# Performance work log

Measured on AMD Instinct MI355X. Metric: run time of the kernel, lower is better.

Reference implementation:

```python
import jax, jax.numpy as jnp
import numpy as np

EPS = 1e-5


def _lstm(x, W_ih, W_hh, b_ih, b_hh):
    # x: [B, T, in]; torch LSTM gate order i, f, g, o. Returns (last h, last c).
    def step(carry, xt):
        h, c = carry
        z = xt @ W_ih.T + h @ W_hh.T + (b_ih + b_hh)  # [B, 4H]
        i, f, g, o = jnp.split(z, 4, axis=-1)
        c = jax.nn.sigmoid(f) * c + jax.nn.sigmoid(i) * jnp.tanh(g)
        h = jax.nn.sigmoid(o) * jnp.tanh(c)
        return (h, c), None
    h0 = jnp.zeros((x.shape[0], W_hh.shape[1]), x.dtype)
    (h, c), _ = jax.lax.scan(step, (h0, h0), jnp.swapaxes(x, 0, 1))
    return h, c


def _bn_train(x, g, b):
    # BatchNorm1d in training mode: batch stats, biased variance.
    m = x.mean(axis=0)
    v = x.var(axis=0)
    return g * (x - m) * jax.lax.rsqrt(v + EPS) + b


def _forward(agent_traj, neighbours, aW_ih, aW_hh, ab_ih, ab_hh,
             nW_ih, nW_hh, nb_ih, nb_hh, dW_ih, dW_hh, db_ih, db_hh,
             pW, pb, rW, rb, m1W, m1b, g1, be1, m2W, m2b, g2, be2,
             i1W, i1b, ig1, ib1, i2W, i2b, ig2, ib2, segment_ids):
    B = agent_traj.shape[0]
    # relative distance: neighbour last position - owning agent's last position
    rel = neighbours[:, -1, :] - agent_traj[segment_ids, -1, :]          # [N, 2]
    agent_h, agent_c = _lstm(agent_traj, aW_ih, aW_hh, ab_ih, ab_hh)     # [B, 64]
    neigh_h, _ = _lstm(neighbours, nW_ih, nW_hh, nb_ih, nb_hh)           # [N, 64]
    rel_emb = rel @ rW.T + rb                                            # [N, 64]
    x = jnp.concatenate([neigh_h, rel_emb], axis=1)                      # [N, 128]
    x = _bn_train(jax.nn.relu(x @ m1W.T + m1b), g1, be1)                 # [N, 512]
    x = _bn_train(jax.nn.relu(x @ m2W.T + m2b), g2, be2)                 # [N, 1024]
    # per-sample max pooling over each sample's neighbours (zeros if none)
    pooled = jax.ops.segment_max(x, segment_ids, num_segments=B)         # [B, 1024]
    counts = jax.ops.segment_sum(jnp.ones((x.shape[0],), x.dtype), segment_ids, num_segments=B)
    pooled = jnp.where(counts[:, None] > 0, pooled, jnp.zeros((), x.dtype))
    d = jnp.concatenate([pooled, agent_h], axis=1)                       # [B, 1088]
    d = _bn_train(jax.nn.relu(d @ i1W.T + i1b), ig1, ib1)                # [B, 1024]
    d = _bn_train(jax.nn.relu(d @ i2W.T + i2b), ig2, ib2)                # [B, 64]

    def dec_step(carry, _):
        h, c = carry
        z = h @ dW_ih.T + h @ dW_hh.T + (db_ih + db_hh)
        i, f, g, o = jnp.split(z, 4, axis=-1)
        c = jax.nn.sigmoid(f) * c + jax.nn.sigmoid(i) * jnp.tanh(g)
        h = jax.nn.sigmoid(o) * jnp.tanh(c)
        return (h, c), h
    _, hs = jax.lax.scan(dec_step, (d, agent_c), None, length=30)        # [30, B, 64]
    pred = jnp.einsum('tbh,oh->bto', hs, pW) + pb                        # [B, 30, 2]
    return pred


def setup_inputs() -> dict:
    B, T, N, Tn, H = 2048, 20, 32768, 20, 64
    key = jax.random.key(0)
    ki = iter(jax.random.split(key, 40))
    def rn(shape, s=0.1):
        return jax.random.normal(next(ki), shape, dtype=jnp.float32) * s
    inp = dict(
        agent_traj=rn((B, T, 2), 1.0),
        neighbours=rn((N, Tn, 2), 1.0),
        aW_ih=rn((4 * H, 2)), aW_hh=rn((4 * H, H)), ab_ih=rn((4 * H,)), ab_hh=rn((4 * H,)),
        nW_ih=rn((4 * H, 2)), nW_hh=rn((4 * H, H)), nb_ih=rn((4 * H,)), nb_hh=rn((4 * H,)),
        dW_ih=rn((4 * H, H)), dW_hh=rn((4 * H, H)), db_ih=rn((4 * H,)), db_hh=rn((4 * H,)),
        pW=rn((2, H)), pb=rn((2,)),
        rW=rn((H, 2)), rb=rn((H,)),
        m1W=rn((512, 128)), m1b=rn((512,)),
        g1=jnp.ones((512,), jnp.float32), be1=jnp.zeros((512,), jnp.float32),
        m2W=rn((1024, 512)), m2b=rn((1024,)),
        g2=jnp.ones((1024,), jnp.float32), be2=jnp.zeros((1024,), jnp.float32),
        i1W=rn((1024, 1088)), i1b=rn((1024,)),
        ig1=jnp.ones((1024,), jnp.float32), ib1=jnp.zeros((1024,), jnp.float32),
        i2W=rn((H, 1024)), i2b=rn((H,)),
        ig2=jnp.ones((H,), jnp.float32), ib2=jnp.zeros((H,), jnp.float32),
        segment_ids=jnp.sort(jax.random.randint(next(ki), (N,), 0, B)).astype(jnp.int32),
    )
    return inp


def reference(agent_traj, neighbours, aW_ih, aW_hh, ab_ih, ab_hh,
              nW_ih, nW_hh, nb_ih, nb_hh, dW_ih, dW_hh, db_ih, db_hh,
              pW, pb, rW, rb, m1W, m1b, g1, be1, m2W, m2b, g2, be2,
              i1W, i1b, ig1, ib1, i2W, i2b, ig2, ib2, segment_ids):
    return _forward(agent_traj, neighbours, aW_ih, aW_hh, ab_ih, ab_hh,
                    nW_ih, nW_hh, nb_ih, nb_hh, dW_ih, dW_hh, db_ih, db_hh,
                    pW, pb, rW, rb, m1W, m1b, g1, be1, m2W, m2b, g2, be2,
                    i1W, i1b, ig1, ib1, i2W, i2b, ig2, ib2, segment_ids)
```

## Files before the change

### kernel.cpp

```cpp
#include <hip/hip_runtime.h>

#define EPS_BN 1e-5f

typedef __attribute__((ext_vector_type(8))) short short8;
typedef __attribute__((ext_vector_type(4))) float f32x4;

__device__ __forceinline__ float fast_rcp(float x) { return __builtin_amdgcn_rcpf(x); }
__device__ __forceinline__ float sigmoid_f(float x) { return fast_rcp(1.0f + __expf(-x)); }
__device__ __forceinline__ float tanh_f(float x) { return 1.0f - 2.0f * fast_rcp(__expf(2.0f * x) + 1.0f); }

__device__ __forceinline__ unsigned short f2bf(float f) {
    unsigned u = __float_as_uint(f);
    u += 0x7FFFu + ((u >> 16) & 1u);
    return (unsigned short)(u >> 16);
}
__device__ __forceinline__ unsigned pk_bf(float a, float b) {
    return (unsigned)f2bf(a) | ((unsigned)f2bf(b) << 16);
}
__device__ __forceinline__ float bf_hi(float f) {
    return __uint_as_float((unsigned)f2bf(f) << 16);
}
__device__ __forceinline__ float bf2f(unsigned short u) {
    return __uint_as_float((unsigned)u << 16);
}

union AFrag { short e[8]; short8 v; };
union BFrag { uint4 u; short8 v; };

__global__ __launch_bounds__(256, 2) void lstm_mfma(
    const float* __restrict__ x,
    const float* __restrict__ W_ih,
    const float* __restrict__ W_hh,
    const float* __restrict__ b_ih,
    const float* __restrict__ b_hh,
    float* __restrict__ h_out,
    float* __restrict__ c_out,
    int T)
{
    __shared__ unsigned h_ex[2][16 * 52];
    __shared__ float z_lds[4 * 64 * 17];

    const int tid  = threadIdx.x;
    const int g    = tid >> 6;
    const int lane = tid & 63;
    const int s    = lane & 15;
    const int q    = lane >> 4;
    const long seq = (long)blockIdx.x * 16 + s;

    short8 ahi[4][3], alo[4][3];
#pragma unroll
    for (int Ti = 0; Ti < 4; ++Ti) {
        const int n = g * 64 + Ti * 16 + s;
#pragma unroll
        for (int kc = 0; kc < 2; ++kc) {
            const float* src = &W_hh[n * 64 + kc * 32 + q * 8];
            float4 v0 = *(const float4*)src;
            float4 v1 = *(const float4*)(src + 4);
            float v[8] = {v0.x, v0.y, v0.z, v0.w, v1.x, v1.y, v1.z, v1.w};
            AFrag a, b;
#pragma unroll
            for (int j = 0; j < 8; ++j) {
                a.e[j] = (short)f2bf(v[j]);
                b.e[j] = (short)f2bf(v[j] - bf_hi(v[j]));
            }
            ahi[Ti][kc] = a.v;
            alo[Ti][kc] = b.v;
        }
        AFrag a2, b2;
#pragma unroll
        for (int j = 0; j < 8; ++j) { a2.e[j] = 0; b2.e[j] = 0; }
        if (q == 0) {
            const float wi0 = W_ih[n * 2 + 0];
            const float wi1 = W_ih[n * 2 + 1];
            const float bs  = b_ih[n] + b_hh[n];
            a2.e[0] = (short)f2bf(wi0); b2.e[0] = (short)f2bf(wi0 - bf_hi(wi0));
            a2.e[1] = (short)f2bf(wi1); b2.e[1] = (short)f2bf(wi1 - bf_hi(wi1));
            a2.e[2] = (short)f2bf(bs);  b2.e[2] = (short)f2bf(bs  - bf_hi(bs));
        }
        ahi[Ti][2] = a2.v;
        alo[Ti][2] = b2.v;
    }

    for (int i = tid; i < 2 * 16 * 52; i += 256) (&h_ex[0][0])[i] = 0u;
    __syncthreads();
    if (tid < 16) {
        h_ex[0][tid * 52 + 33] = pk_bf(1.0f, 0.0f);
        float2 xv = *(const float2*)&x[((long)blockIdx.x * 16 + tid) * (long)(T * 2)];
        h_ex[0][tid * 52 + 32] = pk_bf(xv.x, xv.y);
        h_ex[1][tid * 52 + 32] = pk_bf(xv.x - bf_hi(xv.x), xv.y - bf_hi(xv.y));
    }
    __syncthreads();

    const int jg = tid >> 4;
    const int sc = tid & 15;
    const long seqc = (long)blockIdx.x * 16 + sc;
    float creg[4] = {0.f, 0.f, 0.f, 0.f};

    for (int t = 0; t < T; ++t) {
        BFrag bhi[3], blo[3];
#pragma unroll
        for (int kc = 0; kc < 3; ++kc) {
            const int off = s * 52 + kc * 16 + (q >> 1) * 8 + (q & 1) * 4;
            bhi[kc].u = *(const uint4*)&h_ex[0][off];
            blo[kc].u = *(const uint4*)&h_ex[1][off];
        }

        f32x4 acc[4];
#pragma unroll
        for (int Ti = 0; Ti < 4; ++Ti) acc[Ti] = (f32x4)0.f;

#pragma unroll
        for (int kc = 0; kc < 3; ++kc) {
            const short8 bh = bhi[kc].v;
            const short8 bl = blo[kc].v;
#pragma unroll
            for (int Ti = 0; Ti < 4; ++Ti) {
                f32x4 a = acc[Ti];
                a = __builtin_amdgcn_mfma_f32_16x16x32_bf16(ahi[Ti][kc], bh, a, 0, 0, 0);
                a = __builtin_amdgcn_mfma_f32_16x16x32_bf16(ahi[Ti][kc], bl, a, 0, 0, 0);
                a = __builtin_amdgcn_mfma_f32_16x16x32_bf16(alo[Ti][kc], bh, a, 0, 0, 0);
                acc[Ti] = a;
            }
        }

#pragma unroll
        for (int Ti = 0; Ti < 4; ++Ti)
#pragma unroll
        for (int r = 0; r < 4; ++r)
            z_lds[(g * 64 + Ti * 16 + q * 4 + r) * 17 + s] = acc[Ti][r];
        __syncthreads();

        float hval[4];
#pragma unroll
        for (int r = 0; r < 4; ++r) {
            const int j = jg * 4 + r;
            const float zi = z_lds[(0 * 64 + j) * 17 + sc];
            const float zf = z_lds[(1 * 64 + j) * 17 + sc];
            const float zg = z_lds[(2 * 64 + j) * 17 + sc];
            const float zo = z_lds[(3 * 64 + j) * 17 + sc];
            const float c = fmaf(sigmoid_f(zf), creg[r], sigmoid_f(zi) * tanh_f(zg));
            creg[r] = c;
            hval[r] = sigmoid_f(zo) * tanh_f(c);
        }
        {
            const int j0 = jg * 4;
            const int w0 = sc * 52 + (j0 >> 4) * 8 + ((j0 >> 2) & 3) * 2;
            h_ex[0][w0]     = pk_bf(hval[0], hval[1]);
            h_ex[0][w0 + 1] = pk_bf(hval[2], hval[3]);
            h_ex[1][w0]     = pk_bf(hval[0] - bf_hi(hval[0]), hval[1] - bf_hi(hval[1]));
            h_ex[1][w0 + 1] = pk_bf(hval[2] - bf_hi(hval[2]), hval[3] - bf_hi(hval[3]));
        }
        if (tid < 16 && t + 1 < T) {
            float2 xv = *(const float2*)&x[((long)blockIdx.x * 16 + tid) * (long)(T * 2) + (t + 1) * 2];
            h_ex[0][tid * 52 + 32] = pk_bf(xv.x, xv.y);
            h_ex[1][tid * 52 + 32] = pk_bf(xv.x - bf_hi(xv.x), xv.y - bf_hi(xv.y));
        }
        if (t == T - 1) {
#pragma unroll
            for (int r = 0; r < 4; ++r) {
                h_out[seqc * 64 + jg * 4 + r] = hval[r];
                if (c_out) c_out[seqc * 64 + jg * 4 + r] = creg[r];
            }
        }
        __syncthreads();
    }
}

__global__ __launch_bounds__(256) void build_x0(
    const float* __restrict__ neigh_h, const float* __restrict__ neighbours,
    const float* __restrict__ agent_traj, const int* __restrict__ seg,
    const float* __restrict__ rW, const float* __restrict__ rb,
    unsigned short* __restrict__ x0hi, unsigned short* __restrict__ x0lo, int T)
{
    const long n = (long)blockIdx.x * 2 + (threadIdx.x >> 7);
    const int j = threadIdx.x & 127;
    float v;
    if (j < 64) {
        v = neigh_h[n*64 + j];
    } else {
        const int o = j - 64;
        const int sid = seg[n];
        const float ra = neighbours[n*(long)(T*2) + (T-1)*2 + 0] - agent_traj[(long)sid*(T*2) + (T-1)*2 + 0];
        const float rbv= neighbours[n*(long)(T*2) + (T-1)*2 + 1] - agent_traj[(long)sid*(T*2) + (T-1)*2 + 1];
        v = fmaf(rW[o*2+0], ra, fmaf(rW[o*2+1], rbv, rb[o]));
    }
    x0hi[n*128 + j] = f2bf(v);
    x0lo[n*128 + j] = f2bf(v - bf_hi(v));
}

__global__ __launch_bounds__(64) void prep_wfrag(
    const float* __restrict__ W, const float* __restrict__ sc, int K,
    unsigned short* __restrict__ Whi, unsigned short* __restrict__ Wlo)
{
    const int nKc = K >> 5;
    const int blk = blockIdx.x;
    const int ti = blk / nKc, kc = blk - ti * nKc;
    const int l = threadIdx.x;
    const int n = ti * 16 + (l & 15);
    const int k0 = kc * 32 + (l >> 4) * 8;
    const long ob = ((long)blk * 64 + l) * 8;
#pragma unroll
    for (int j = 0; j < 8; ++j) {
        float v = W[(long)n * K + k0 + j];
        if (sc) v *= sc[k0 + j];
        Whi[ob + j] = f2bf(v);
        Wlo[ob + j] = f2bf(v - bf_hi(v));
    }
}

__global__ __launch_bounds__(64) void prep_bias(
    const float* __restrict__ W, const float* __restrict__ sh,
    const float* __restrict__ b, int K, float* __restrict__ bout)
{
    const int n = blockIdx.x;
    const int l = threadIdx.x;
    float s = 0.f;
    if (sh)
        for (int k = l; k < K; k += 64) s += sh[k] * W[(long)n * K + k];
#pragma unroll
    for (int m = 32; m >= 1; m >>= 1) s += __shfl_xor(s, m, 64);
    if (l == 0) bout[n] = b[n] + s;
}

__global__ __launch_bounds__(256, 2) void gemm_split(
    const unsigned short* __restrict__ Ahi,
    const unsigned short* __restrict__ Alo,
    const unsigned short* __restrict__ Whi,
    const unsigned short* __restrict__ Wlo,
    const float* __restrict__ bias,
    float* __restrict__ Yf,
    unsigned short* __restrict__ Yhi,
    unsigned short* __restrict__ Ylo,
    float* __restrict__ accum,
    int M, int K, int O)
{
    __shared__ unsigned short As[2][128 * 56];
    const int t = threadIdx.x;
    const int lane = t & 63;
    const int w = t >> 6;
    const int wm = w & 1, wn = w >> 1;
    const int m0 = blockIdx.y * 128, n0 = blockIdx.x * 128;
    const int nKc = K >> 5;

    f32x4 acc[4][4];
#pragma unroll
    for (int mt = 0; mt < 4; ++mt)
#pragma unroll
    for (int nt = 0; nt < 4; ++nt) acc[mt][nt] = (f32x4)0.f;

    const long aoff = (long)(m0 + (t >> 1)) * K + (t & 1) * 16;
    const unsigned short* aph = Ahi + aoff;
    const unsigned short* apl = Alo + aoff;
    const int so = (t >> 1) * 56 + (t & 1) * 16;
    const int arow = wm * 64 + (lane & 15);
    const int acol = (lane >> 4) * 8;
    const long bt0 = (long)((n0 >> 4) + wn * 4);

    uint4 rah0, rah1, ral0, ral1;
    auto loadAreg = [&](int kc) {
        rah0 = *(const uint4*)(aph + kc * 32);
        rah1 = *(const uint4*)(aph + kc * 32 + 8);
        ral0 = *(const uint4*)(apl + kc * 32);
        ral1 = *(const uint4*)(apl + kc * 32 + 8);
    };
    auto storeAs = [&]() {
        *(uint4*)&As[0][so] = rah0; *(uint4*)&As[0][so + 8] = rah1;
        *(uint4*)&As[1][so] = ral0; *(uint4*)&As[1][so + 8] = ral1;
    };
    auto loadB = [&](BFrag* bh, BFrag* bl, int kc) {
#pragma unroll
        for (int nt = 0; nt < 4; ++nt) {
            const long fb = ((bt0 + nt) * nKc + kc) * 512 + lane * 8;
            bh[nt].u = *(const uint4*)(Whi + fb);
            bl[nt].u = *(const uint4*)(Wlo + fb);
        }
    };
    auto compute = [&](BFrag* bh, BFrag* bl) {
        BFrag afh[4], afl[4];
#pragma unroll
        for (int mt = 0; mt < 4; ++mt) {
            afh[mt].u = *(const uint4*)&As[0][(arow + mt * 16) * 56 + acol];
            afl[mt].u = *(const uint4*)&As[1][(arow + mt * 16) * 56 + acol];
        }
#pragma unroll
        for (int nt = 0; nt < 4; ++nt)
#pragma unroll
        for (int mt = 0; mt < 4; ++mt) {
            f32x4 a = acc[mt][nt];
            a = __builtin_amdgcn_mfma_f32_16x16x32_bf16(afh[mt].v, bh[nt].v, a, 0, 0, 0);
            a = __builtin_amdgcn_mfma_f32_16x16x32_bf16(afh[mt].v, bl[nt].v, a, 0, 0, 0);
            a = __builtin_amdgcn_mfma_f32_16x16x32_bf16(afl[mt].v, bh[nt].v, a, 0, 0, 0);
            acc[mt][nt] = a;
        }
    };

    BFrag bh0[4], bl0[4], bh1[4], bl1[4];
    loadAreg(0);
    loadB(bh0, bl0, 0);
    for (int kc = 0; kc < nKc; kc += 2) {
        __syncthreads();
        storeAs();
        loadAreg(kc + 1);
        __syncthreads();
        loadB(bh1, bl1, kc + 1);
        compute(bh0, bl0);
        __syncthreads();
        storeAs();
        if (kc + 2 < nKc) loadAreg(kc + 2);
        __syncthreads();
        if (kc + 2 < nKc) loadB(bh0, bl0, kc + 2);
        compute(bh1, bl1);
    }

    const int cn = lane & 15, cq = lane >> 4;
#pragma unroll
    for (int nt = 0; nt < 4; ++nt) {
        const int n = n0 + wn * 64 + nt * 16 + cn;
        const float bs = bias[n];
        float s = 0.f, ssq = 0.f;
#pragma unroll
        for (int mt = 0; mt < 4; ++mt)
#pragma unroll
        for (int r = 0; r < 4; ++r) {
            const long m = m0 + wm * 64 + mt * 16 + cq * 4 + r;
            const float v = fmaxf(acc[mt][nt][r] + bs, 0.f);
            s += v; ssq += v * v;
            if (Yf) {
                Yf[m * O + n] = v;
            } else {
                Yhi[m * O + n] = f2bf(v);
                Ylo[m * O + n] = f2bf(v - bf_hi(v));
            }
        }
        if (accum) {
            s   += __shfl_xor(s, 16, 64);   ssq += __shfl_xor(ssq, 16, 64);
            s   += __shfl_xor(s, 32, 64);   ssq += __shfl_xor(ssq, 32, 64);
            if (cq == 0) {
                atomicAdd(&accum[n], s);
                atomicAdd(&accum[O + n], ssq);
            }
        }
    }
}

__global__ __launch_bounds__(256) void colstats(
    const float* __restrict__ Y, int M, int O, int chunkRows,
    float* __restrict__ accum)
{
    const int c = blockIdx.x * 64 + (threadIdx.x & 63);
    const int rgrp = threadIdx.x >> 6;
    const int r0 = blockIdx.y * chunkRows;
    int rend = r0 + chunkRows; if (rend > M) rend = M;
    float s = 0.f, ss = 0.f;
    for (int r = r0 + rgrp; r < rend; r += 4) {
        const float v = Y[(long)r*O + c];
        s += v; ss += v*v;
    }
    __shared__ float l1[256], l2[256];
    l1[threadIdx.x] = s; l2[threadIdx.x] = ss;
    __syncthreads();
    if (threadIdx.x < 64) {
        const int c2 = blockIdx.x * 64 + threadIdx.x;
        s  = l1[threadIdx.x] + l1[threadIdx.x+64] + l1[threadIdx.x+128] + l1[threadIdx.x+192];
        ss = l2[threadIdx.x] + l2[threadIdx.x+64] + l2[threadIdx.x+128] + l2[threadIdx.x+192];
        atomicAdd(&accum[c2], s);
        atomicAdd(&accum[O + c2], ss);
    }
}

__global__ __launch_bounds__(256) void bn_finalize(
    const float* __restrict__ accum, const float* __restrict__ g,
    const float* __restrict__ be, int O, float invM,
    float* __restrict__ scale, float* __restrict__ shift)
{
    const int o = blockIdx.x * 256 + threadIdx.x;
    if (o < O) {
        const float mean = accum[o] * invM;
        const float var  = accum[O + o] * invM - mean * mean;
        const float sc   = g[o] * rsqrtf(var + EPS_BN);
        scale[o] = sc;
        shift[o] = be[o] - mean * sc;
    }
}

__global__ __launch_bounds__(256) void segmax_kernel(
    const float* __restrict__ Y , const int* __restrict__ seg,
    const float* __restrict__ scale, const float* __restrict__ shift,
    int N, float* __restrict__ pooled )
{
    const int b = blockIdx.x;
    int l = 0, h = N;
    while (l < h) { const int mid = (l + h) >> 1; if (seg[mid] < b) l = mid + 1; else h = mid; }
    const int lo = l;
    h = N;
    while (l < h) { const int mid = (l + h) >> 1; if (seg[mid] < b + 1) l = mid + 1; else h = mid; }
    const int hi = l;

    for (int cc = threadIdx.x; cc < 1024; cc += 256) {
        float m;
        if (lo >= hi) {
            m = 0.0f;
        } else {
            m = -3.4e38f;
            for (int r = lo; r < hi; ++r) m = fmaxf(m, Y[(long)r*1024 + cc]);
            m = fmaf(scale[cc], m, shift[cc]);
        }
        pooled[(long)b*1024 + cc] = m;
    }
}

__global__ __launch_bounds__(256) void build_d0(
    const float* __restrict__ pooled, const float* __restrict__ agent_h,
    unsigned short* __restrict__ d0hi, unsigned short* __restrict__ d0lo)
{
    const int b = blockIdx.x;
    for (int c = threadIdx.x; c < 1088; c += 256) {
        const float v = (c < 1024) ? pooled[(long)b*1024 + c]
                                   : agent_h[(long)b*64 + (c - 1024)];
        d0hi[(long)b*1088 + c] = f2bf(v);
        d0lo[(long)b*1088 + c] = f2bf(v - bf_hi(v));
    }
}

__global__ __launch_bounds__(256) void gemm_i2_part(
    const float* __restrict__ A,
    const float* __restrict__ W,
    const float* __restrict__ ascale, const float* __restrict__ ashift,
    float* __restrict__ part, int M, int K, int kchunk)
{
    __shared__ float As[16][132];
    __shared__ float Bs[16][68];
    const int t = threadIdx.x;
    const int m0 = blockIdx.x * 128;
    const int ks = blockIdx.y;
    const int kbeg = ks * kchunk;
    const int kend = kbeg + kchunk;
    const int tm = (t & 15) * 8;
    const int tn = (t >> 4) * 4;
    const int ar = t >> 1;
    const int ac = (t & 1) * 8;
    const int br = t >> 2;
    const int bc = (t & 3) * 4;

    float acc[8][4];
#pragma unroll
    for (int i = 0; i < 8; ++i)
#pragma unroll
    for (int j = 0; j < 4; ++j) acc[i][j] = 0.f;

    for (int k0 = kbeg; k0 < kend; k0 += 16) {
        float4 a0 = *(const float4*)&A[(long)(m0+ar)*K + k0 + ac];
        float4 a1 = *(const float4*)&A[(long)(m0+ar)*K + k0 + ac + 4];
        float4 s0 = *(const float4*)&ascale[k0 + ac];
        float4 s1 = *(const float4*)&ascale[k0 + ac + 4];
        float4 h0 = *(const float4*)&ashift[k0 + ac];
        float4 h1 = *(const float4*)&ashift[k0 + ac + 4];
        a0.x = fmaf(a0.x, s0.x, h0.x); a0.y = fmaf(a0.y, s0.y, h0.y);
        a0.z = fmaf(a0.z, s0.z, h0.z); a0.w = fmaf(a0.w, s0.w, h0.w);
        a1.x = fmaf(a1.x, s1.x, h1.x); a1.y = fmaf(a1.y, s1.y, h1.y);
        a1.z = fmaf(a1.z, s1.z, h1.z); a1.w = fmaf(a1.w, s1.w, h1.w);
        float4 b0 = *(const float4*)&W[(long)br*K + k0 + bc];
        __syncthreads();
        As[ac+0][ar] = a0.x; As[ac+1][ar] = a0.y; As[ac+2][ar] = a0.z; As[ac+3][ar] = a0.w;
        As[ac+4][ar] = a1.x; As[ac+5][ar] = a1.y; As[ac+6][ar] = a1.z; As[ac+7][ar] = a1.w;
        Bs[bc+0][br] = b0.x; Bs[bc+1][br] = b0.y; Bs[bc+2][br] = b0.z; Bs[bc+3][br] = b0.w;
        __syncthreads();
#pragma unroll
        for (int kk = 0; kk < 16; ++kk) {
            float av[8], bv[4];
            *(float4*)&av[0] = *(const float4*)&As[kk][tm];
            *(float4*)&av[4] = *(const float4*)&As[kk][tm + 4];
            *(float4*)&bv[0] = *(const float4*)&Bs[kk][tn];
#pragma unroll
            for (int i = 0; i < 8; ++i)
#pragma unroll
            for (int j = 0; j < 4; ++j)
                acc[i][j] = fmaf(av[i], bv[j], acc[i][j]);
        }
    }

    float* po = part + (long)ks * M * 64;
#pragma unroll
    for (int i = 0; i < 8; ++i)
        *(float4*)&po[(long)(m0 + tm + i) * 64 + tn] = *(float4*)&acc[i][0];
}

__global__ __launch_bounds__(256) void i2_finish(
    const float* __restrict__ part, const float* __restrict__ bias,
    int M, int KS, float* __restrict__ t2)
{
    const long idx = (long)blockIdx.x * 256 + threadIdx.x;
    if (idx < (long)M * 64) {
        float s = 0.f;
        for (int ks = 0; ks < KS; ++ks) s += part[(long)ks * M * 64 + idx];
        t2[idx] = fmaxf(s + bias[idx & 63], 0.f);
    }
}

__global__ __launch_bounds__(256) void prep_dec(
    const float* __restrict__ dW_ih, const float* __restrict__ dW_hh,
    const float* __restrict__ db_ih, const float* __restrict__ db_hh,
    float* __restrict__ Wc, float* __restrict__ bc)
{
    const int idx = blockIdx.x * 256 + threadIdx.x;
    if (idx < 256*64) Wc[idx] = dW_ih[idx] + dW_hh[idx];
    else if (idx < 256*64 + 256) bc[idx - 256*64] = db_ih[idx - 256*64] + db_hh[idx - 256*64];
}

__global__ __launch_bounds__(256) void decoder_kernel(
    const float* __restrict__ t2, const float* __restrict__ sc4,
    const float* __restrict__ sh4, const float* __restrict__ agent_c,
    const float* __restrict__ Wc, const float* __restrict__ bc,
    const float* __restrict__ pW, const float* __restrict__ pb,
    float* __restrict__ pred )
{
    __shared__ float h_lds[2][64];
    __shared__ float zg_lds[2][64];
    __shared__ float zo_lds[2][64];
    const int t = threadIdx.x;
    const int lane = t & 63;
    const int wave = t >> 6;
    const int s = wave >> 1;
    const int role = wave & 1;
    const long seq = (long)blockIdx.x * 2 + s;

    const int r0 = role * 128 + lane;
    const int r1 = r0 + 64;
    float w0[64], w1[64];
#pragma unroll
    for (int k = 0; k < 64; k += 4) {
        float4 va = *(const float4*)&Wc[r0 * 64 + k];
        w0[k] = va.x; w0[k+1] = va.y; w0[k+2] = va.z; w0[k+3] = va.w;
        float4 vb = *(const float4*)&Wc[r1 * 64 + k];
        w1[k] = vb.x; w1[k+1] = vb.y; w1[k+2] = vb.z; w1[k+3] = vb.w;
    }
    const float bias0 = bc[r0];
    const float bias1 = bc[r1];
    const float pw0 = pW[lane], pw1 = pW[64 + lane];
    const float pb0 = pb[0], pb1 = pb[1];

    float c = agent_c[seq*64 + lane];
    if (role == 0)
        h_lds[s][lane] = fmaf(sc4[lane], t2[seq*64 + lane], sh4[lane]);
    __syncthreads();
    float hv = h_lds[s][lane];

    for (int step = 0; step < 30; ++step) {
        float z0 = bias0, z1 = bias1;
#pragma unroll
        for (int k = 0; k < 64; ++k) {
            float hk = __int_as_float(__builtin_amdgcn_readlane(__float_as_int(hv), k));
            z0 = fmaf(hk, w0[k], z0);
            z1 = fmaf(hk, w1[k], z1);
        }
        if (role == 1) { zg_lds[s][lane] = z0; zo_lds[s][lane] = z1; }
        __syncthreads();
        if (role == 0) {
            const float ig = sigmoid_f(z0);
            const float fg = sigmoid_f(z1);
            const float gg = tanh_f(zg_lds[s][lane]);
            const float og = sigmoid_f(zo_lds[s][lane]);
            c = fmaf(fg, c, ig * gg);
            h_lds[s][lane] = og * tanh_f(c);
        }
        __syncthreads();
        hv = h_lds[s][lane];
        if (role == 0) {
            float p0 = hv * pw0;
            float p1 = hv * pw1;
#pragma unroll
            for (int m = 32; m >= 1; m >>= 1) {
                p0 += __shfl_xor(p0, m, 64);
                p1 += __shfl_xor(p1, m, 64);
            }
            if (lane == 0) {
                pred[seq*60 + step*2 + 0] = p0 + pb0;
                pred[seq*60 + step*2 + 1] = p1 + pb1;
            }
        }
    }
}

extern "C" void kernel_launch(void* const* d_in, const int* in_sizes, int n_in,
                              void* d_out, int out_size, void* d_ws, size_t ws_size,
                              hipStream_t stream)
{
    const float* agent_traj = (const float*)d_in[0];
    const float* neighbours = (const float*)d_in[1];
    const float* aW_ih = (const float*)d_in[2];
    const float* aW_hh = (const float*)d_in[3];
    const float* ab_ih = (const float*)d_in[4];
    const float* ab_hh = (const float*)d_in[5];
    const float* nW_ih = (const float*)d_in[6];
    const float* nW_hh = (const float*)d_in[7];
    const float* nb_ih = (const float*)d_in[8];
    const float* nb_hh = (const float*)d_in[9];
    const float* dW_ih = (const float*)d_in[10];
    const float* dW_hh = (const float*)d_in[11];
    const float* db_ih = (const float*)d_in[12];
    const float* db_hh = (const float*)d_in[13];
    const float* pW = (const float*)d_in[14];
    const float* pb = (const float*)d_in[15];
    const float* rW = (const float*)d_in[16];
    const float* rb = (const float*)d_in[17];
    const float* m1W = (const float*)d_in[18];
    const float* m1b = (const float*)d_in[19];
    const float* g1  = (const float*)d_in[20];
    const float* be1 = (const float*)d_in[21];
    const float* m2W = (const float*)d_in[22];
    const float* m2b = (const float*)d_in[23];
    const float* g2  = (const float*)d_in[24];
    const float* be2 = (const float*)d_in[25];
    const float* i1W = (const float*)d_in[26];
    const float* i1b = (const float*)d_in[27];
    const float* ig1 = (const float*)d_in[28];
    const float* ib1 = (const float*)d_in[29];
    const float* i2W = (const float*)d_in[30];
    const float* i2b = (const float*)d_in[31];
    const float* ig2 = (const float*)d_in[32];
    const float* ib2 = (const float*)d_in[33];
    const int*   seg = (const int*)d_in[34];
    float* pred = (float*)d_out;

    const int B = 2048, T = 20, N = 32768;

    char* p = (char*)d_ws;
    auto alloc = [&](size_t bytes) -> char* {
        char* r = p; p += (bytes + 255) & ~(size_t)255; return r;
    };
    float* agent_h = (float*)alloc((size_t)B*64*4);
    float* agent_c = (float*)alloc((size_t)B*64*4);
    char* neigh_region = alloc((size_t)N*64*4);
    char* x0hi_region  = alloc((size_t)N*128*2);
    unsigned short* x0lo = (unsigned short*)alloc((size_t)N*128*2);
    char* y1hi_region  = alloc((size_t)N*512*2);
    unsigned short* y1lo = (unsigned short*)alloc((size_t)N*512*2);
    float* y2 = (float*)alloc((size_t)N*1024*4);
    float* accAll = (float*)alloc((size_t)(1024+2048+2048+128)*4);
    float* acc1 = accAll;
    float* acc2 = accAll + 1024;
    float* acc3 = accAll + 3072;
    float* acc4 = accAll + 5120;
    float* sc1 = (float*)alloc(512*4);  float* sh1 = (float*)alloc(512*4);
    float* sc2 = (float*)alloc(1024*4); float* sh2 = (float*)alloc(1024*4);
    float* sc3 = (float*)alloc(1024*4); float* sh3 = (float*)alloc(1024*4);
    float* sc4 = (float*)alloc(64*4);   float* sh4 = (float*)alloc(64*4);
    float* Wc = (float*)alloc(256*64*4);
    float* bc = (float*)alloc(256*4);
    unsigned short* W1hi = (unsigned short*)alloc((size_t)512*128*2);
    unsigned short* W1lo = (unsigned short*)alloc((size_t)512*128*2);
    unsigned short* W2hi = (unsigned short*)alloc((size_t)1024*512*2);
    unsigned short* W2lo = (unsigned short*)alloc((size_t)1024*512*2);
    unsigned short* Wi1hi = (unsigned short*)alloc((size_t)1024*1088*2);
    unsigned short* Wi1lo = (unsigned short*)alloc((size_t)1024*1088*2);
    float* b1f = (float*)alloc(512*4);
    float* b2f = (float*)alloc(1024*4);
    float* bi1f = (float*)alloc(1024*4);
    float* i2part = (float*)alloc((size_t)8*B*64*4);

    float* neigh_h = (float*)neigh_region;
    float* t1      = (float*)neigh_region;
    unsigned short* x0hi = (unsigned short*)x0hi_region;
    float* pooled  = (float*)x0hi_region;
    unsigned short* y1hi = (unsigned short*)y1hi_region;
    unsigned short* d0hi = (unsigned short*)y1hi_region;
    unsigned short* d0lo = d0hi + (size_t)B*1088;
    float* t2 = (float*)(y1hi_region + (size_t)2*B*1088*2);

    hipMemsetAsync(accAll, 0, (1024+2048+2048+128)*sizeof(float), stream);

    prep_wfrag<<<(512/16)*(128/32), 64, 0, stream>>>(m1W, nullptr, 128, W1hi, W1lo);
    prep_bias<<<512, 64, 0, stream>>>(m1W, nullptr, m1b, 128, b1f);
    prep_wfrag<<<(1024/16)*(1088/32), 64, 0, stream>>>(i1W, nullptr, 1088, Wi1hi, Wi1lo);
    prep_bias<<<1024, 64, 0, stream>>>(i1W, nullptr, i1b, 1088, bi1f);
    prep_dec<<<65, 256, 0, stream>>>(dW_ih, dW_hh, db_ih, db_hh, Wc, bc);

    lstm_mfma<<<B/16, 256, 0, stream>>>(agent_traj, aW_ih, aW_hh, ab_ih, ab_hh,
                                        agent_h, agent_c, T);
    lstm_mfma<<<N/16, 256, 0, stream>>>(neighbours, nW_ih, nW_hh, nb_ih, nb_hh,
                                        neigh_h, nullptr, T);
    build_x0<<<N/2, 256, 0, stream>>>(neigh_h, neighbours, agent_traj, seg, rW, rb,
                                      x0hi, x0lo, T);

    gemm_split<<<dim3(512/128, N/128), 256, 0, stream>>>(
        x0hi, x0lo, W1hi, W1lo, b1f, nullptr, y1hi, y1lo, acc1, N, 128, 512);
    bn_finalize<<<2, 256, 0, stream>>>(acc1, g1, be1, 512, 1.0f/N, sc1, sh1);

    prep_wfrag<<<(1024/16)*(512/32), 64, 0, stream>>>(m2W, sc1, 512, W2hi, W2lo);
    prep_bias<<<1024, 64, 0, stream>>>(m2W, sh1, m2b, 512, b2f);

    gemm_split<<<dim3(1024/128, N/128), 256, 0, stream>>>(
        y1hi, y1lo, W2hi, W2lo, b2f, y2, nullptr, nullptr, acc2, N, 512, 1024);
    bn_finalize<<<4, 256, 0, stream>>>(acc2, g2, be2, 1024, 1.0f/N, sc2, sh2);

    segmax_kernel<<<B, 256, 0, stream>>>(y2, seg, sc2, sh2, N, pooled);
    build_d0<<<B, 256, 0, stream>>>(pooled, agent_h, d0hi, d0lo);

    gemm_split<<<dim3(1024/128, B/128), 256, 0, stream>>>(
        d0hi, d0lo, Wi1hi, Wi1lo, bi1f, t1, nullptr, nullptr, acc3, B, 1088, 1024);
    bn_finalize<<<4, 256, 0, stream>>>(acc3, ig1, ib1, 1024, 1.0f/B, sc3, sh3);

    gemm_i2_part<<<dim3(B/128, 8), 256, 0, stream>>>(t1, i2W, sc3, sh3, i2part,
                                                     B, 1024, 128);
    i2_finish<<<(B*64)/256, 256, 0, stream>>>(i2part, i2b, B, 8, t2);
    colstats<<<dim3(1, 8), 256, 0, stream>>>(t2, B, 64, 256, acc4);
    bn_finalize<<<1, 256, 0, stream>>>(acc4, ig2, ib2, 64, 1.0f/B, sc4, sh4);

    decoder_kernel<<<B/2, 256, 0, stream>>>(t2, sc4, sh4, agent_c, Wc, bc, pW, pb, pred);
}
```

Before: 675.1 us.

## Fuse per-segment max pooling into second MLP GEMM epilogue via atomicMax

```diff
diff --git a/kernel.cpp b/kernel.cpp
--- a/kernel.cpp
+++ b/kernel.cpp
@@ -45,7 +45,6 @@
     const int lane = tid & 63;
     const int s    = lane & 15;
     const int q    = lane >> 4;
-    const long seq = (long)blockIdx.x * 16 + s;
 
     short8 ahi[4][3], alo[4][3];
 #pragma unroll
@@ -232,9 +231,12 @@
     unsigned short* __restrict__ Yhi,
     unsigned short* __restrict__ Ylo,
     float* __restrict__ accum,
+    const int* __restrict__ segp,
+    float* __restrict__ poolmax,
     int M, int K, int O)
 {
     __shared__ unsigned short As[2][128 * 56];
+    __shared__ int segl[128];
     const int t = threadIdx.x;
     const int lane = t & 63;
     const int w = t >> 6;
@@ -312,6 +314,12 @@
         compute(bh1, bl1);
     }
 
+    if (segp) {
+        __syncthreads();
+        if (t < 128) segl[t] = segp[m0 + t];
+        __syncthreads();
+    }
+
     const int cn = lane & 15, cq = lane >> 4;
 #pragma unroll
     for (int nt = 0; nt < 4; ++nt) {
@@ -319,18 +327,32 @@
         const float bs = bias[n];
         float s = 0.f, ssq = 0.f;
 #pragma unroll
-        for (int mt = 0; mt < 4; ++mt)
-#pragma unroll
-        for (int r = 0; r < 4; ++r) {
-            const long m = m0 + wm * 64 + mt * 16 + cq * 4 + r;
-            const float v = fmaxf(acc[mt][nt][r] + bs, 0.f);
-            s += v; ssq += v * v;
-            if (Yf) {
-                Yf[m * O + n] = v;
-            } else {
-                Yhi[m * O + n] = f2bf(v);
-                Ylo[m * O + n] = f2bf(v - bf_hi(v));
+        for (int mt = 0; mt < 4; ++mt) {
+            const int mb = wm * 64 + mt * 16 + cq * 4;
+            float vmax = 0.f; int sid = -1;
+#pragma unroll
+            for (int r = 0; r < 4; ++r) {
+                const float v = fmaxf(acc[mt][nt][r] + bs, 0.f);
+                s += v; ssq += v * v;
+                if (segp) {
+                    const int sr = segl[mb + r];
+                    if (r == 0) { vmax = v; sid = sr; }
+                    else if (sr == sid) { vmax = fmaxf(vmax, v); }
+                    else {
+                        if (vmax > 0.f)
+                            atomicMax((int*)&poolmax[(long)sid * O + n], __float_as_int(vmax));
+                        sid = sr; vmax = v;
+                    }
+                } else if (Yf) {
+                    Yf[(long)(m0 + mb + r) * O + n] = v;
+                } else {
+                    const long idx = (long)(m0 + mb + r) * O + n;
+                    Yhi[idx] = f2bf(v);
+                    Ylo[idx] = f2bf(v - bf_hi(v));
+                }
             }
+            if (segp && vmax > 0.f)
+                atomicMax((int*)&poolmax[(long)sid * O + n], __float_as_int(vmax));
         }
         if (accum) {
             s   += __shfl_xor(s, 16, 64);   ssq += __shfl_xor(ssq, 16, 64);
@@ -383,40 +405,23 @@
     }
 }
 
-__global__ __launch_bounds__(256) void segmax_kernel(
-    const float* __restrict__ Y , const int* __restrict__ seg,
-    const float* __restrict__ scale, const float* __restrict__ shift,
-    int N, float* __restrict__ pooled )
+__global__ __launch_bounds__(256) void build_d0(
+    const float* __restrict__ poolraw, const float* __restrict__ agent_h,
+    const int* __restrict__ seg, int N,
+    const float* __restrict__ sc2, const float* __restrict__ sh2,
+    unsigned short* __restrict__ d0hi, unsigned short* __restrict__ d0lo)
 {
     const int b = blockIdx.x;
     int l = 0, h = N;
     while (l < h) { const int mid = (l + h) >> 1; if (seg[mid] < b) l = mid + 1; else h = mid; }
-    const int lo = l;
-    h = N;
-    while (l < h) { const int mid = (l + h) >> 1; if (seg[mid] < b + 1) l = mid + 1; else h = mid; }
-    const int hi = l;
-
-    for (int cc = threadIdx.x; cc < 1024; cc += 256) {
-        float m;
-        if (lo >= hi) {
-            m = 0.0f;
+    const bool nonempty = (l < N) && (seg[l] == b);
+    for (int c = threadIdx.x; c < 1088; c += 256) {
+        float v;
+        if (c < 1024) {
+            v = nonempty ? fmaf(sc2[c], poolraw[(long)b*1024 + c], sh2[c]) : 0.f;
         } else {
-            m = -3.4e38f;
-            for (int r = lo; r < hi; ++r) m = fmaxf(m, Y[(long)r*1024 + cc]);
-            m = fmaf(scale[cc], m, shift[cc]);
-        }
-        pooled[(long)b*1024 + cc] = m;
-    }
-}
-
-__global__ __launch_bounds__(256) void build_d0(
-    const float* __restrict__ pooled, const float* __restrict__ agent_h,
-    unsigned short* __restrict__ d0hi, unsigned short* __restrict__ d0lo)
-{
-    const int b = blockIdx.x;
-    for (int c = threadIdx.x; c < 1088; c += 256) {
-        const float v = (c < 1024) ? pooled[(long)b*1024 + c]
-                                   : agent_h[(long)b*64 + (c - 1024)];
+            v = agent_h[(long)b*64 + (c - 1024)];
+        }
         d0hi[(long)b*1088 + c] = f2bf(v);
         d0lo[(long)b*1088 + c] = f2bf(v - bf_hi(v));
     }
@@ -631,11 +636,11 @@
     float* agent_h = (float*)alloc((size_t)B*64*4);
     float* agent_c = (float*)alloc((size_t)B*64*4);
     char* neigh_region = alloc((size_t)N*64*4);
-    char* x0hi_region  = alloc((size_t)N*128*2);
+    unsigned short* x0hi = (unsigned short*)alloc((size_t)N*128*2);
     unsigned short* x0lo = (unsigned short*)alloc((size_t)N*128*2);
     char* y1hi_region  = alloc((size_t)N*512*2);
     unsigned short* y1lo = (unsigned short*)alloc((size_t)N*512*2);
-    float* y2 = (float*)alloc((size_t)N*1024*4);
+    float* poolraw = (float*)alloc((size_t)B*1024*4);
     float* accAll = (float*)alloc((size_t)(1024+2048+2048+128)*4);
     float* acc1 = accAll;
     float* acc2 = accAll + 1024;
@@ -660,14 +665,13 @@
 
     float* neigh_h = (float*)neigh_region;
     float* t1      = (float*)neigh_region;
-    unsigned short* x0hi = (unsigned short*)x0hi_region;
-    float* pooled  = (float*)x0hi_region;
     unsigned short* y1hi = (unsigned short*)y1hi_region;
     unsigned short* d0hi = (unsigned short*)y1hi_region;
     unsigned short* d0lo = d0hi + (size_t)B*1088;
     float* t2 = (float*)(y1hi_region + (size_t)2*B*1088*2);
 
     hipMemsetAsync(accAll, 0, (1024+2048+2048+128)*sizeof(float), stream);
+    hipMemsetAsync(poolraw, 0, (size_t)B*1024*4, stream);
 
     prep_wfrag<<<(512/16)*(128/32), 64, 0, stream>>>(m1W, nullptr, 128, W1hi, W1lo);
     prep_bias<<<512, 64, 0, stream>>>(m1W, nullptr, m1b, 128, b1f);
@@ -683,21 +687,23 @@
                                       x0hi, x0lo, T);
 
     gemm_split<<<dim3(512/128, N/128), 256, 0, stream>>>(
-        x0hi, x0lo, W1hi, W1lo, b1f, nullptr, y1hi, y1lo, acc1, N, 128, 512);
+        x0hi, x0lo, W1hi, W1lo, b1f, nullptr, y1hi, y1lo, acc1,
+        nullptr, nullptr, N, 128, 512);
     bn_finalize<<<2, 256, 0, stream>>>(acc1, g1, be1, 512, 1.0f/N, sc1, sh1);
 
     prep_wfrag<<<(1024/16)*(512/32), 64, 0, stream>>>(m2W, sc1, 512, W2hi, W2lo);
     prep_bias<<<1024, 64, 0, stream>>>(m2W, sh1, m2b, 512, b2f);
 
     gemm_split<<<dim3(1024/128, N/128), 256, 0, stream>>>(
-        y1hi, y1lo, W2hi, W2lo, b2f, y2, nullptr, nullptr, acc2, N, 512, 1024);
+        y1hi, y1lo, W2hi, W2lo, b2f, nullptr, nullptr, nullptr, acc2,
+        seg, poolraw, N, 512, 1024);
     bn_finalize<<<4, 256, 0, stream>>>(acc2, g2, be2, 1024, 1.0f/N, sc2, sh2);
 
-    segmax_kernel<<<B, 256, 0, stream>>>(y2, seg, sc2, sh2, N, pooled);
-    build_d0<<<B, 256, 0, stream>>>(pooled, agent_h, d0hi, d0lo);
+    build_d0<<<B, 256, 0, stream>>>(poolraw, agent_h, seg, N, sc2, sh2, d0hi, d0lo);
 
     gemm_split<<<dim3(1024/128, B/128), 256, 0, stream>>>(
-        d0hi, d0lo, Wi1hi, Wi1lo, bi1f, t1, nullptr, nullptr, acc3, B, 1088, 1024);
+        d0hi, d0lo, Wi1hi, Wi1lo, bi1f, t1, nullptr, nullptr, acc3,
+        nullptr, nullptr, B, 1088, 1024);
     bn_finalize<<<4, 256, 0, stream>>>(acc3, ig1, ib1, 1024, 1.0f/B, sc3, sh3);
 
     gemm_i2_part<<<dim3(B/128, 8), 256, 0, stream>>>(t1, i2W, sc3, sh3, i2part,
```

New measurement: 659.8 us. 2.3% less time.
